# Kernel tuning notes

Hardware: AMD Instinct MI355X
Metric: run time of the kernel (lower is better)

Reference implementation:

```python
import jax, jax.numpy as jnp
import numpy as np

B, S, IN, OUT, E, K = 4, 2048, 4096, 4096, 8, 16
POOLS = E * K  # 128 rank-one pools


def setup_inputs() -> dict:
    key = jax.random.key(0)
    k1, k2, k3, k4, k5 = jax.random.split(key, 5)
    sc = 0.02
    return {
        "hidden_states": jax.random.normal(k1, (B, S, IN), jnp.float32),
        "w0": jax.random.normal(k2, (OUT, IN), jnp.float32) * sc,   # pretrained Linear weight
        "b0": jnp.zeros((OUT,), jnp.float32),                        # pretrained Linear bias
        "wr": jax.random.normal(k3, (POOLS, IN), jnp.float32) * sc,  # Router stacked v.T
        "u": jax.random.normal(k4, (OUT, POOLS), jnp.float32) * sc,  # RankOnePools.u
        "svh": jax.random.normal(k5, (POOLS, IN), jnp.float32) * sc, # RankOnePools.svh
        "top_k": 2,
    }


def reference(hidden_states, w0, b0, wr, u, svh, top_k):
    # pretrained dense path (expert_use_diff=True)
    pretrained_out = jnp.einsum('bsi,oi->bso', hidden_states, w0) + b0

    x = hidden_states.reshape(-1, hidden_states.shape[-1])  # [N, IN]

    # Router: logits over num_experts*k rank-one pools
    logits = jnp.einsum('ni,pi->np', x, wr)                  # [N, POOLS]
    vals, idx = jax.lax.top_k(logits, top_k)                 # [N, top_k]
    vals = vals / jnp.sum(vals, axis=-1, keepdims=True)      # computed but UNUSED (matches original torch code)

    # RankOnePools: gather selected rank-one factors and combine
    svh_sel = svh[idx]                                       # [N, top_k, IN]
    dot = jnp.einsum('ni,nti->nt', x, svh_sel)               # [N, top_k]
    u_sel = u.T[idx]                                         # [N, top_k, OUT]
    expert_out = jnp.einsum('nt,nto->no', dot, u_sel)        # [N, OUT]

    out = pretrained_out + expert_out.reshape(pretrained_out.shape)
    return out
```

## Files before the change

kernel.cpp:

```cpp
#include <hip/hip_runtime.h>

#define K_DIM  4096
#define N_OUT  4096
#define N_TOK  8192
#define N_POOL 128

typedef __bf16 bf16x8 __attribute__((ext_vector_type(8)));
typedef float  f32x4  __attribute__((ext_vector_type(4)));
typedef unsigned short u16x8 __attribute__((ext_vector_type(8)));

__device__ __forceinline__ unsigned short f2bf(float f) {
    union { float f; unsigned u; } v; v.f = f;
    unsigned r = v.u + 0x7fffu + ((v.u >> 16) & 1u);
    return (unsigned short)(r >> 16);
}
__device__ __forceinline__ float bf2f(unsigned short b) {
    union { unsigned u; float f; } v; v.u = ((unsigned)b) << 16;
    return v.f;
}

__global__ __launch_bounds__(256) void k_convert_w0(const float* __restrict__ w0,
                                                    unsigned short* __restrict__ w0b) {
    size_t base = ((size_t)blockIdx.x * 256 + threadIdx.x) * 8;
    float4 a = *(const float4*)(w0 + base);
    float4 b = *(const float4*)(w0 + base + 4);
    u16x8 r;
    r[0] = f2bf(a.x); r[1] = f2bf(a.y); r[2] = f2bf(a.z); r[3] = f2bf(a.w);
    r[4] = f2bf(b.x); r[5] = f2bf(b.y); r[6] = f2bf(b.z); r[7] = f2bf(b.w);
    *(u16x8*)(w0b + base) = r;
}

__global__ __launch_bounds__(256) void k_transpose_u(const float* __restrict__ u,
                                                     float* __restrict__ uT) {
    __shared__ float t[32][65];
    const int o0 = blockIdx.x * 64, p0 = blockIdx.y * 32;
    const int tid = threadIdx.x;
#pragma unroll
    for (int it = 0; it < 8; it++) {
        int o = (tid >> 5) + it * 8;
        t[tid & 31][o] = u[(size_t)(o0 + o) * N_POOL + p0 + (tid & 31)];
    }
    __syncthreads();
#pragma unroll
    for (int it = 0; it < 8; it++) {
        int p = (tid >> 6) + it * 4;
        uT[(size_t)(p0 + p) * N_OUT + o0 + (tid & 63)] = t[p][tid & 63];
    }
}

#define RT_TOK 32
#define RT_BK  32
#define WR_LD  132

__global__ __launch_bounds__(256) void k_router(const float* __restrict__ x,
                                                const float* __restrict__ wr,
                                                const float* __restrict__ svh,
                                                unsigned short* __restrict__ xb,
                                                int* __restrict__ idxp,
                                                float* __restrict__ dotp) {
    __shared__ float x_lds[RT_TOK][RT_BK];
    __shared__ float wr_lds[RT_BK][WR_LD];
    __shared__ float logits[RT_TOK][N_POOL + 1];
    __shared__ int   sel[RT_TOK][2];

    const int tid = threadIdx.x;
    const int m0  = blockIdx.x * RT_TOK;
    const int pg  = tid & 31;
    const int tg  = tid >> 5;

    const int xtok = tid >> 3, xk = (tid & 7) * 4;

    float acc[4][4] = {};
    float4 x_pf;
    float4 wr_pf[4];

    x_pf = *(const float4*)(x + (size_t)(m0 + xtok) * K_DIM + xk);
#pragma unroll
    for (int i = 0; i < 4; i++) {
        int cc = tid + 256 * i, p = cc >> 3, kq = (cc & 7) * 4;
        wr_pf[i] = *(const float4*)(wr + (size_t)p * K_DIM + kq);
    }

    for (int t = 0; t < K_DIM / RT_BK; t++) {
        const int k0 = t * RT_BK;
        __syncthreads();
        *(float4*)&x_lds[xtok][xk] = x_pf;
        {
            ushort4 bb;
            bb.x = f2bf(x_pf.x); bb.y = f2bf(x_pf.y); bb.z = f2bf(x_pf.z); bb.w = f2bf(x_pf.w);
            *(ushort4*)(xb + (size_t)(m0 + xtok) * K_DIM + k0 + xk) = bb;
        }
#pragma unroll
        for (int i = 0; i < 4; i++) {
            int cc = tid + 256 * i, p = cc >> 3, kq = (cc & 7) * 4;
            wr_lds[kq + 0][p] = wr_pf[i].x; wr_lds[kq + 1][p] = wr_pf[i].y;
            wr_lds[kq + 2][p] = wr_pf[i].z; wr_lds[kq + 3][p] = wr_pf[i].w;
        }
        __syncthreads();
        if (t + 1 < K_DIM / RT_BK) {
            const int kn = k0 + RT_BK;
            x_pf = *(const float4*)(x + (size_t)(m0 + xtok) * K_DIM + kn + xk);
#pragma unroll
            for (int i = 0; i < 4; i++) {
                int cc = tid + 256 * i, p = cc >> 3, kq = (cc & 7) * 4;
                wr_pf[i] = *(const float4*)(wr + (size_t)p * K_DIM + kn + kq);
            }
        }
#pragma unroll
        for (int kk = 0; kk < RT_BK; kk += 4) {
            float4 xr[4];
#pragma unroll
            for (int tt = 0; tt < 4; tt++) xr[tt] = *(float4*)&x_lds[tg * 4 + tt][kk];
#pragma unroll
            for (int j = 0; j < 4; j++) {
                float4 wv = *(float4*)&wr_lds[kk + j][pg * 4];
#pragma unroll
                for (int tt = 0; tt < 4; tt++) {
                    float a = (&xr[tt].x)[j];
                    acc[tt][0] += a * wv.x; acc[tt][1] += a * wv.y;
                    acc[tt][2] += a * wv.z; acc[tt][3] += a * wv.w;
                }
            }
        }
    }

    __syncthreads();
#pragma unroll
    for (int tt = 0; tt < 4; tt++)
#pragma unroll
        for (int q = 0; q < 4; q++)
            logits[tg * 4 + tt][pg * 4 + q] = acc[tt][q];
    __syncthreads();

    if (tid < RT_TOK) {
        float v1 = -3.4e38f, v2 = -3.4e38f; int i1 = 0, i2 = 0;
        for (int p = 0; p < N_POOL; p++) {
            float v = logits[tid][p];
            if (v > v1)      { v2 = v1; i2 = i1; v1 = v; i1 = p; }
            else if (v > v2) { v2 = v;  i2 = p; }
        }
        sel[tid][0] = i1; sel[tid][1] = i2;
        idxp[(size_t)(m0 + tid) * 2 + 0] = i1;
        idxp[(size_t)(m0 + tid) * 2 + 1] = i2;
    }
    __syncthreads();

    const int wave = tid >> 6, lane = tid & 63;
    for (int s = wave; s < RT_TOK; s += 4) {
        const size_t n = (size_t)(m0 + s);
        const int e0 = sel[s][0], e1 = sel[s][1];
        float d0 = 0.f, d1 = 0.f;
#pragma unroll
        for (int it = 0; it < 8; it++) {
            const int e = (it * 64 + lane) * 8;
            u16x8 xv = *(const u16x8*)(xb + n * K_DIM + e);
            float4 s0 = *(const float4*)(svh + (size_t)e0 * K_DIM + e);
            float4 s1 = *(const float4*)(svh + (size_t)e0 * K_DIM + e + 4);
            float4 s2 = *(const float4*)(svh + (size_t)e1 * K_DIM + e);
            float4 s3 = *(const float4*)(svh + (size_t)e1 * K_DIM + e + 4);
            float x0 = bf2f(xv[0]), x1 = bf2f(xv[1]), x2 = bf2f(xv[2]), x3 = bf2f(xv[3]);
            float x4 = bf2f(xv[4]), x5 = bf2f(xv[5]), x6 = bf2f(xv[6]), x7 = bf2f(xv[7]);
            d0 += x0*s0.x + x1*s0.y + x2*s0.z + x3*s0.w + x4*s1.x + x5*s1.y + x6*s1.z + x7*s1.w;
            d1 += x0*s2.x + x1*s2.y + x2*s2.z + x3*s2.w + x4*s3.x + x5*s3.y + x6*s3.z + x7*s3.w;
        }
#pragma unroll
        for (int off = 32; off > 0; off >>= 1) {
            d0 += __shfl_down(d0, off);
            d1 += __shfl_down(d1, off);
        }
        if (lane == 0) { dotp[n * 2 + 0] = d0; dotp[n * 2 + 1] = d1; }
    }
}

__global__ __launch_bounds__(256) void k_gemm(const unsigned short* __restrict__ xb,
                                              const unsigned short* __restrict__ w0b,
                                              const float* __restrict__ b0,
                                              const float* __restrict__ uT,
                                              const int* __restrict__ idxp,
                                              const float* __restrict__ dotp,
                                              float* __restrict__ out) {
    __shared__ unsigned short Als[128 * 64];
    __shared__ unsigned short Bls[128 * 64];

    const int tid  = threadIdx.x;
    const int lane = tid & 63;
    const int wv   = tid >> 6;
    const int wm   = wv & 1, wn = wv >> 1;
    const int lrow = lane & 15, lquad = lane >> 4;
    const size_t m0 = (size_t)blockIdx.y * 128;
    const size_t n0 = (size_t)blockIdx.x * 128;

    const int srow   = tid >> 3;
    const int xchunk = (tid & 7) ^ (srow & 7);
    const unsigned short* ag = xb  + (m0 + srow) * K_DIM + xchunk * 8;
    const unsigned short* bg = w0b + (n0 + srow) * K_DIM + xchunk * 8;
    unsigned short* al = Als + tid * 8;
    unsigned short* bl = Bls + tid * 8;

    f32x4 acc[4][4] = {};

    for (int k0 = 0; k0 < K_DIM; k0 += 64) {
        __syncthreads();
#pragma unroll
        for (int i = 0; i < 4; i++) {
            __builtin_amdgcn_global_load_lds(
                (const __attribute__((address_space(1))) void*)(ag + (size_t)i * 32 * K_DIM + k0),
                (__attribute__((address_space(3))) void*)(al + i * 2048), 16, 0, 0);
            __builtin_amdgcn_global_load_lds(
                (const __attribute__((address_space(1))) void*)(bg + (size_t)i * 32 * K_DIM + k0),
                (__attribute__((address_space(3))) void*)(bl + i * 2048), 16, 0, 0);
        }
        __syncthreads();
#pragma unroll
        for (int ks = 0; ks < 2; ks++) {
            bf16x8 af[4], bfr[4];
#pragma unroll
            for (int t = 0; t < 4; t++)
                af[t] = *(const bf16x8*)&Als[(wm * 64 + t * 16 + lrow) * 64 +
                                             (((ks * 4 + lquad) ^ (lrow & 7)) * 8)];
#pragma unroll
            for (int t = 0; t < 4; t++)
                bfr[t] = *(const bf16x8*)&Bls[(wn * 64 + t * 16 + lrow) * 64 +
                                              (((ks * 4 + lquad) ^ (lrow & 7)) * 8)];
#pragma unroll
            for (int mt = 0; mt < 4; mt++)
#pragma unroll
                for (int nt = 0; nt < 4; nt++)
                    acc[mt][nt] = __builtin_amdgcn_mfma_f32_16x16x32_bf16(af[mt], bfr[nt], acc[mt][nt], 0, 0, 0);
        }
    }

#pragma unroll
    for (int mt = 0; mt < 4; mt++) {
        const size_t rb = m0 + wm * 64 + mt * 16 + lquad * 4;
#pragma unroll
        for (int r = 0; r < 4; r++) {
            const size_t gm = rb + r;
            const int e0 = idxp[gm * 2 + 0], e1 = idxp[gm * 2 + 1];
            const float dd0 = dotp[gm * 2 + 0], dd1 = dotp[gm * 2 + 1];
#pragma unroll
            for (int nt = 0; nt < 4; nt++) {
                const size_t gn = n0 + wn * 64 + nt * 16 + lrow;
                float vv = acc[mt][nt][r] + b0[gn]
                         + dd0 * uT[(size_t)e0 * N_OUT + gn] + dd1 * uT[(size_t)e1 * N_OUT + gn];
                out[gm * N_OUT + gn] = vv;
            }
        }
    }
}

extern "C" void kernel_launch(void* const* d_in, const int* in_sizes, int n_in,
                              void* d_out, int out_size, void* d_ws, size_t ws_size,
                              hipStream_t stream) {
    const float* x   = (const float*)d_in[0];
    const float* w0  = (const float*)d_in[1];
    const float* b0  = (const float*)d_in[2];
    const float* wr  = (const float*)d_in[3];
    const float* u   = (const float*)d_in[4];
    const float* svh = (const float*)d_in[5];
    float* out = (float*)d_out;

    char* ws = (char*)d_ws;
    unsigned short* xb  = (unsigned short*)ws;
    unsigned short* w0b = (unsigned short*)(ws + 67108864);
    int*   idxp = (int*)(ws + 100663296);
    float* dotp = (float*)(ws + 100663296 + 65536);
    float* uTp  = (float*)(ws + 100663296 + 131072);

    k_convert_w0<<<dim3(16777216 / (256 * 8)), dim3(256), 0, stream>>>(w0, w0b);
    k_transpose_u<<<dim3(N_OUT / 64, N_POOL / 32), dim3(256), 0, stream>>>(u, uTp);
    k_router<<<dim3(N_TOK / RT_TOK), dim3(256), 0, stream>>>(x, wr, svh, xb, idxp, dotp);
    k_gemm<<<dim3(N_OUT / 128, N_TOK / 128), dim3(256), 0, stream>>>(xb, w0b, b0, uTp, idxp, dotp, out);
}
```

Measured before the change: 722.3 us.

## Restructure router to register-tiled global loads with wave-level top-2 reduction

The router kernel no longer stages x and wr through LDS. Each wave now handles 4 tokens, with each lane streaming transposed wr (produced by a new transpose kernel) and x rows straight from global memory into register accumulators. Top-2 selection moves from a serial per-thread scan over LDS logits to a shuffle-based butterfly reduction. The selected-pool dot product now reads fp32 x instead of bf16 x. The x-to-bf16 conversion moves out of the router into a separate generic convert kernel. This frees LDS and removes the block syncs, at the cost of an extra full read of x and no shared reuse of wr across waves, which relies on the cache.

```diff
diff --git a/kernel.cpp b/kernel.cpp
--- a/kernel.cpp
+++ b/kernel.cpp
@@ -14,20 +14,16 @@
     unsigned r = v.u + 0x7fffu + ((v.u >> 16) & 1u);
     return (unsigned short)(r >> 16);
 }
-__device__ __forceinline__ float bf2f(unsigned short b) {
-    union { unsigned u; float f; } v; v.u = ((unsigned)b) << 16;
-    return v.f;
-}
-
-__global__ __launch_bounds__(256) void k_convert_w0(const float* __restrict__ w0,
-                                                    unsigned short* __restrict__ w0b) {
+
+__global__ __launch_bounds__(256) void k_convert(const float* __restrict__ src,
+                                                 unsigned short* __restrict__ dst) {
     size_t base = ((size_t)blockIdx.x * 256 + threadIdx.x) * 8;
-    float4 a = *(const float4*)(w0 + base);
-    float4 b = *(const float4*)(w0 + base + 4);
+    float4 a = *(const float4*)(src + base);
+    float4 b = *(const float4*)(src + base + 4);
     u16x8 r;
     r[0] = f2bf(a.x); r[1] = f2bf(a.y); r[2] = f2bf(a.z); r[3] = f2bf(a.w);
     r[4] = f2bf(b.x); r[5] = f2bf(b.y); r[6] = f2bf(b.z); r[7] = f2bf(b.w);
-    *(u16x8*)(w0b + base) = r;
+    *(u16x8*)(dst + base) = r;
 }
 
 __global__ __launch_bounds__(256) void k_transpose_u(const float* __restrict__ u,
@@ -48,127 +44,139 @@
     }
 }
 
-#define RT_TOK 32
-#define RT_BK  32
-#define WR_LD  132
+__global__ __launch_bounds__(256) void k_transpose_wr(const float* __restrict__ wr,
+                                                      float* __restrict__ wrT) {
+    __shared__ float t[32][33];
+    const int k0 = blockIdx.x * 32, p0 = blockIdx.y * 32;
+    const int tid = threadIdx.x;
+#pragma unroll
+    for (int it = 0; it < 4; it++) {
+        int p = (tid >> 5) + it * 8;
+        int k = tid & 31;
+        t[k][p] = wr[(size_t)(p0 + p) * K_DIM + k0 + k];
+    }
+    __syncthreads();
+#pragma unroll
+    for (int it = 0; it < 4; it++) {
+        int k = (tid >> 5) + it * 8;
+        int p = tid & 31;
+        wrT[(size_t)(k0 + k) * N_POOL + p0 + p] = t[k][p];
+    }
+}
+
+#define RTOK 16
 
 __global__ __launch_bounds__(256) void k_router(const float* __restrict__ x,
-                                                const float* __restrict__ wr,
+                                                const float* __restrict__ wrT,
                                                 const float* __restrict__ svh,
-                                                unsigned short* __restrict__ xb,
                                                 int* __restrict__ idxp,
                                                 float* __restrict__ dotp) {
-    __shared__ float x_lds[RT_TOK][RT_BK];
-    __shared__ float wr_lds[RT_BK][WR_LD];
-    __shared__ float logits[RT_TOK][N_POOL + 1];
-    __shared__ int   sel[RT_TOK][2];
-
-    const int tid = threadIdx.x;
-    const int m0  = blockIdx.x * RT_TOK;
-    const int pg  = tid & 31;
-    const int tg  = tid >> 5;
-
-    const int xtok = tid >> 3, xk = (tid & 7) * 4;
-
-    float acc[4][4] = {};
-    float4 x_pf;
-    float4 wr_pf[4];
-
-    x_pf = *(const float4*)(x + (size_t)(m0 + xtok) * K_DIM + xk);
-#pragma unroll
-    for (int i = 0; i < 4; i++) {
-        int cc = tid + 256 * i, p = cc >> 3, kq = (cc & 7) * 4;
-        wr_pf[i] = *(const float4*)(wr + (size_t)p * K_DIM + kq);
-    }
-
-    for (int t = 0; t < K_DIM / RT_BK; t++) {
-        const int k0 = t * RT_BK;
+    const int tid  = threadIdx.x;
+    const int w    = tid >> 6, lane = tid & 63;
+    const int pg   = lane & 31, tg = lane >> 5;
+    const int m0   = blockIdx.x * RTOK;
+    const int tokA = m0 + w * 4 + tg * 2;
+
+    const float* xA = x + (size_t)tokA * K_DIM;
+    const float* xB = xA + K_DIM;
+    const float* wp = wrT + pg * 4;
+
+    float a0[4] = {0.f,0.f,0.f,0.f}, a1[4] = {0.f,0.f,0.f,0.f};
+
+    for (int kc = 0; kc < K_DIM; kc += 256) {
+        for (int k0 = kc; k0 < kc + 256; k0 += 8) {
+            float4 xa[2], xb4[2], wv[8];
+#pragma unroll
+            for (int q = 0; q < 2; q++) {
+                xa[q]  = *(const float4*)(xA + k0 + q * 4);
+                xb4[q] = *(const float4*)(xB + k0 + q * 4);
+            }
+#pragma unroll
+            for (int j = 0; j < 8; j++)
+                wv[j] = *(const float4*)(wp + (size_t)(k0 + j) * N_POOL);
+#pragma unroll
+            for (int q = 0; q < 2; q++)
+#pragma unroll
+                for (int j = 0; j < 4; j++) {
+                    float av = (&xa[q].x)[j], bv = (&xb4[q].x)[j];
+                    float4 wj = wv[q * 4 + j];
+                    a0[0] += av * wj.x; a0[1] += av * wj.y;
+                    a0[2] += av * wj.z; a0[3] += av * wj.w;
+                    a1[0] += bv * wj.x; a1[1] += bv * wj.y;
+                    a1[2] += bv * wj.z; a1[3] += bv * wj.w;
+                }
+        }
         __syncthreads();
-        *(float4*)&x_lds[xtok][xk] = x_pf;
-        {
-            ushort4 bb;
-            bb.x = f2bf(x_pf.x); bb.y = f2bf(x_pf.y); bb.z = f2bf(x_pf.z); bb.w = f2bf(x_pf.w);
-            *(ushort4*)(xb + (size_t)(m0 + xtok) * K_DIM + k0 + xk) = bb;
-        }
-#pragma unroll
-        for (int i = 0; i < 4; i++) {
-            int cc = tid + 256 * i, p = cc >> 3, kq = (cc & 7) * 4;
-            wr_lds[kq + 0][p] = wr_pf[i].x; wr_lds[kq + 1][p] = wr_pf[i].y;
-            wr_lds[kq + 2][p] = wr_pf[i].z; wr_lds[kq + 3][p] = wr_pf[i].w;
-        }
-        __syncthreads();
-        if (t + 1 < K_DIM / RT_BK) {
-            const int kn = k0 + RT_BK;
-            x_pf = *(const float4*)(x + (size_t)(m0 + xtok) * K_DIM + kn + xk);
-#pragma unroll
-            for (int i = 0; i < 4; i++) {
-                int cc = tid + 256 * i, p = cc >> 3, kq = (cc & 7) * 4;
-                wr_pf[i] = *(const float4*)(wr + (size_t)p * K_DIM + kn + kq);
+    }
+
+    float v1[2], v2[2]; int i1[2], i2[2];
+#pragma unroll
+    for (int t = 0; t < 2; t++) {
+        const float* ac = t ? a1 : a0;
+        float b1 = -3.4e38f, b2 = -3.4e38f; int j1 = 0, j2 = 0;
+#pragma unroll
+        for (int q = 0; q < 4; q++) {
+            float v = ac[q]; int idx = pg * 4 + q;
+            if (v > b1)      { b2 = b1; j2 = j1; b1 = v; j1 = idx; }
+            else if (v > b2) { b2 = v;  j2 = idx; }
+        }
+        v1[t] = b1; i1[t] = j1; v2[t] = b2; i2[t] = j2;
+    }
+#pragma unroll
+    for (int off = 1; off < 32; off <<= 1) {
+#pragma unroll
+        for (int t = 0; t < 2; t++) {
+            float o1 = __shfl_xor(v1[t], off), o2 = __shfl_xor(v2[t], off);
+            int  oi1 = __shfl_xor(i1[t], off), oi2 = __shfl_xor(i2[t], off);
+            bool owin = (o1 > v1[t]) || (o1 == v1[t] && oi1 < i1[t]);
+            float n1, n2; int ni1, ni2;
+            if (owin) {
+                n1 = o1; ni1 = oi1;
+                bool sw = (v1[t] > o2) || (v1[t] == o2 && i1[t] < oi2);
+                n2 = sw ? v1[t] : o2; ni2 = sw ? i1[t] : oi2;
+            } else {
+                n1 = v1[t]; ni1 = i1[t];
+                bool sw = (o1 > v2[t]) || (o1 == v2[t] && oi1 < i2[t]);
+                n2 = sw ? o1 : v2[t]; ni2 = sw ? oi1 : i2[t];
             }
-        }
-#pragma unroll
-        for (int kk = 0; kk < RT_BK; kk += 4) {
-            float4 xr[4];
-#pragma unroll
-            for (int tt = 0; tt < 4; tt++) xr[tt] = *(float4*)&x_lds[tg * 4 + tt][kk];
-#pragma unroll
-            for (int j = 0; j < 4; j++) {
-                float4 wv = *(float4*)&wr_lds[kk + j][pg * 4];
-#pragma unroll
-                for (int tt = 0; tt < 4; tt++) {
-                    float a = (&xr[tt].x)[j];
-                    acc[tt][0] += a * wv.x; acc[tt][1] += a * wv.y;
-                    acc[tt][2] += a * wv.z; acc[tt][3] += a * wv.w;
-                }
-            }
-        }
-    }
-
-    __syncthreads();
-#pragma unroll
-    for (int tt = 0; tt < 4; tt++)
-#pragma unroll
-        for (int q = 0; q < 4; q++)
-            logits[tg * 4 + tt][pg * 4 + q] = acc[tt][q];
-    __syncthreads();
-
-    if (tid < RT_TOK) {
-        float v1 = -3.4e38f, v2 = -3.4e38f; int i1 = 0, i2 = 0;
-        for (int p = 0; p < N_POOL; p++) {
-            float v = logits[tid][p];
-            if (v > v1)      { v2 = v1; i2 = i1; v1 = v; i1 = p; }
-            else if (v > v2) { v2 = v;  i2 = p; }
-        }
-        sel[tid][0] = i1; sel[tid][1] = i2;
-        idxp[(size_t)(m0 + tid) * 2 + 0] = i1;
-        idxp[(size_t)(m0 + tid) * 2 + 1] = i2;
-    }
-    __syncthreads();
-
-    const int wave = tid >> 6, lane = tid & 63;
-    for (int s = wave; s < RT_TOK; s += 4) {
-        const size_t n = (size_t)(m0 + s);
-        const int e0 = sel[s][0], e1 = sel[s][1];
+            v1[t] = n1; i1[t] = ni1; v2[t] = n2; i2[t] = ni2;
+        }
+    }
+    if ((lane & 31) == 0) {
+#pragma unroll
+        for (int t = 0; t < 2; t++) {
+            idxp[(size_t)(tokA + t) * 2 + 0] = i1[t];
+            idxp[(size_t)(tokA + t) * 2 + 1] = i2[t];
+        }
+    }
+
+#pragma unroll
+    for (int s = 0; s < 4; s++) {
+        const int src = (s >> 1) * 32;
+        const int e0 = __shfl((s & 1) ? i1[1] : i1[0], src);
+        const int e1 = __shfl((s & 1) ? i2[1] : i2[0], src);
+        const float* xr = x   + (size_t)(m0 + w * 4 + s) * K_DIM;
+        const float* p0 = svh + (size_t)e0 * K_DIM;
+        const float* p1 = svh + (size_t)e1 * K_DIM;
         float d0 = 0.f, d1 = 0.f;
-#pragma unroll
-        for (int it = 0; it < 8; it++) {
-            const int e = (it * 64 + lane) * 8;
-            u16x8 xv = *(const u16x8*)(xb + n * K_DIM + e);
-            float4 s0 = *(const float4*)(svh + (size_t)e0 * K_DIM + e);
-            float4 s1 = *(const float4*)(svh + (size_t)e0 * K_DIM + e + 4);
-            float4 s2 = *(const float4*)(svh + (size_t)e1 * K_DIM + e);
-            float4 s3 = *(const float4*)(svh + (size_t)e1 * K_DIM + e + 4);
-            float x0 = bf2f(xv[0]), x1 = bf2f(xv[1]), x2 = bf2f(xv[2]), x3 = bf2f(xv[3]);
-            float x4 = bf2f(xv[4]), x5 = bf2f(xv[5]), x6 = bf2f(xv[6]), x7 = bf2f(xv[7]);
-            d0 += x0*s0.x + x1*s0.y + x2*s0.z + x3*s0.w + x4*s1.x + x5*s1.y + x6*s1.z + x7*s1.w;
-            d1 += x0*s2.x + x1*s2.y + x2*s2.z + x3*s2.w + x4*s3.x + x5*s3.y + x6*s3.z + x7*s3.w;
+#pragma unroll 4
+        for (int it = 0; it < 16; it++) {
+            const int off = (it * 64 + lane) * 4;
+            float4 xv = *(const float4*)(xr + off);
+            float4 q0 = *(const float4*)(p0 + off);
+            float4 q1 = *(const float4*)(p1 + off);
+            d0 += xv.x*q0.x + xv.y*q0.y + xv.z*q0.z + xv.w*q0.w;
+            d1 += xv.x*q1.x + xv.y*q1.y + xv.z*q1.z + xv.w*q1.w;
         }
 #pragma unroll
         for (int off = 32; off > 0; off >>= 1) {
             d0 += __shfl_down(d0, off);
             d1 += __shfl_down(d1, off);
         }
-        if (lane == 0) { dotp[n * 2 + 0] = d0; dotp[n * 2 + 1] = d1; }
+        if (lane == 0) {
+            dotp[(size_t)(m0 + w * 4 + s) * 2 + 0] = d0;
+            dotp[(size_t)(m0 + w * 4 + s) * 2 + 1] = d1;
+        }
     }
 }
 
@@ -264,11 +272,14 @@
     unsigned short* xb  = (unsigned short*)ws;
     unsigned short* w0b = (unsigned short*)(ws + 67108864);
     int*   idxp = (int*)(ws + 100663296);
-    float* dotp = (float*)(ws + 100663296 + 65536);
-    float* uTp  = (float*)(ws + 100663296 + 131072);
-
-    k_convert_w0<<<dim3(16777216 / (256 * 8)), dim3(256), 0, stream>>>(w0, w0b);
+    float* dotp = (float*)(ws + 100728832);
+    float* uTp  = (float*)(ws + 100794368);
+    float* wrTp = (float*)(ws + 102891520);
+
+    k_transpose_wr<<<dim3(K_DIM / 32, N_POOL / 32), dim3(256), 0, stream>>>(wr, wrTp);
+    k_router<<<dim3(N_TOK / RTOK), dim3(256), 0, stream>>>(x, wrTp, svh, idxp, dotp);
+    k_convert<<<dim3((N_TOK * K_DIM) / 2048), dim3(256), 0, stream>>>(x, xb);
+    k_convert<<<dim3((N_OUT * K_DIM) / 2048), dim3(256), 0, stream>>>(w0, w0b);
     k_transpose_u<<<dim3(N_OUT / 64, N_POOL / 32), dim3(256), 0, stream>>>(u, uTp);
-    k_router<<<dim3(N_TOK / RT_TOK), dim3(256), 0, stream>>>(x, wr, svh, xb, idxp, dotp);
     k_gemm<<<dim3(N_OUT / 128, N_TOK / 128), dim3(256), 0, stream>>>(xb, w0b, b0, uTp, idxp, dotp, out);
 }
```

Measured after the change: 1.010 ms. +39.8%, slower.
